# Kernel tuning notes

Hardware: AMD Instinct MI355X
Metric: run time of the kernel (lower is better)

## Reference

```python
import jax, jax.numpy as jnp
import numpy as np

EPS = 1e-5
B, N = 16, 131072

def _bn(x, g, b, m, v):
    # x: [C, N]; inference-mode batchnorm with given stats
    return g[:, None] * (x - m[:, None]) * jax.lax.rsqrt(v[:, None] + EPS) + b[:, None]

def _make_npts():
    base = N // B
    offs = np.linspace(-2048, 2048, B).astype(np.int64)
    npts = np.full(B, base, dtype=np.int64) + offs
    npts[-1] += N - npts.sum()
    assert npts.sum() == N and (npts > 0).all()
    return npts

def setup_inputs() -> dict:
    key = jax.random.key(0)
    ks = jax.random.split(key, 16)
    d = {}
    d["x"] = jax.random.normal(ks[0], (3, N), jnp.float32)
    d["npts"] = jnp.asarray(_make_npts(), jnp.int32)
    def w(k, o, i):
        return jax.random.normal(k, (o, i), jnp.float32) * (1.0 / np.sqrt(i))
    def bnp(k, c):
        k1, k2, k3, k4 = jax.random.split(k, 4)
        return (1.0 + 0.1 * jax.random.normal(k1, (c,), jnp.float32),
                0.1 * jax.random.normal(k2, (c,), jnp.float32),
                0.1 * jax.random.normal(k3, (c,), jnp.float32),
                0.5 + jax.random.uniform(k4, (c,), jnp.float32))
    d["W1"] = w(ks[1], 128, 3);   d["b1"] = jnp.zeros(128, jnp.float32)
    d["g1"], d["be1"], d["m1"], d["v1"] = bnp(ks[2], 128)
    d["W2"] = w(ks[3], 256, 128); d["b2"] = jnp.zeros(256, jnp.float32)
    d["g2"], d["be2"], d["m2"], d["v2"] = bnp(ks[4], 256)
    d["W3"] = w(ks[5], 512, 512); d["b3"] = jnp.zeros(512, jnp.float32)
    d["g3"], d["be3"], d["m3"], d["v3"] = bnp(ks[6], 512)
    d["W4"] = w(ks[7], 1024, 512); d["b4"] = jnp.zeros(1024, jnp.float32)
    d["g4"], d["be4"], d["m4"], d["v4"] = bnp(ks[8], 1024)
    return d

def reference(x, npts,
              W1, b1, g1, be1, m1, v1,
              W2, b2, g2, be2, m2, v2,
              W3, b3, g3, be3, m3, v3,
              W4, b4, g4, be4, m4, v4):
    # segment ids for the ragged point->cloud mapping (replaces torch.split loops)
    seg = jnp.repeat(jnp.arange(B, dtype=jnp.int32), npts, total_repeat_length=N)  # [N]
    h = jax.nn.relu(_bn(W1 @ x + b1[:, None], g1, be1, m1, v1))        # [128, N]
    f = _bn(W2 @ h + b2[:, None], g2, be2, m2, v2)                      # [256, N]
    g = jax.ops.segment_max(f.T, seg, num_segments=B)                   # [B, 256]
    gs = g[seg].T                                                       # [256, N] broadcast back
    xc = jnp.concatenate([gs, f], axis=0)                               # [512, N]
    h3 = jax.nn.relu(_bn(W3 @ xc + b3[:, None], g3, be3, m3, v3))       # [512, N]
    h4 = _bn(W4 @ h3 + b4[:, None], g4, be4, m4, v4)                    # [1024, N]
    v = jax.ops.segment_max(h4.T, seg, num_segments=B)                  # [B, 1024]
    return v
```

## Files before the change

kernel.cpp:

```cpp
#include <hip/hip_runtime.h>
#include <hip/hip_bf16.h>
#include <stdint.h>

#define NTOT 131072
#define NSEG 16
#define EPSV 1e-5f

typedef __attribute__((ext_vector_type(8))) short bf16x8;
typedef __attribute__((ext_vector_type(4))) float f32x4;

struct Args {
  const float* x; const int* npts;
  const float *W1,*b1,*g1,*be1,*m1,*v1;
  const float *W2,*b2,*g2,*be2,*m2,*v2;
  const float *W3,*b3,*g3,*be3,*m3,*v3;
  const float *W4,*b4,*g4,*be4,*m4,*v4;
  int* offs;
  float *a1,*c1,*a2,*c2,*a3,*c3,*a4,*c4;
  unsigned int *gkeys,*vkeys;
  unsigned short *w2b;
  unsigned short *w3p;
  unsigned short *w4p;
  unsigned short *fbufp;
  unsigned short *h3p;
  float* cseg;
  float* out;
};

__device__ inline unsigned int f2key(float f){ unsigned u=__float_as_uint(f); return (u&0x80000000u)? ~u : (u|0x80000000u); }
__device__ inline float key2f(unsigned k){ unsigned u=(k&0x80000000u)? (k^0x80000000u) : ~k; return __uint_as_float(u); }
__device__ inline unsigned short f2bf(float f){ __hip_bfloat16 h=__float2bfloat16(f); return *(unsigned short*)&h; }

__device__ inline void gl16(const void* g, void* l){
  __builtin_amdgcn_global_load_lds((const __attribute__((address_space(1))) unsigned int*)g,
                                   (__attribute__((address_space(3))) unsigned int*)l, 16, 0, 0);
}

__global__ void k_setup(Args A){
  int tid = threadIdx.x;
  if (tid==0){ int s=0; A.offs[0]=0; for (int i=0;i<NSEG;i++){ s+=A.npts[i]; A.offs[i+1]=s; } }
  for (int c=tid;c<128;c+=256){ float a=A.g1[c]*rsqrtf(A.v1[c]+EPSV); A.a1[c]=a; A.c1[c]=A.be1[c]+a*(A.b1[c]-A.m1[c]); }
  for (int c=tid;c<256;c+=256){ float a=A.g2[c]*rsqrtf(A.v2[c]+EPSV); A.a2[c]=a; A.c2[c]=A.be2[c]+a*(A.b2[c]-A.m2[c]); }
  for (int c=tid;c<512;c+=256){ float a=A.g3[c]*rsqrtf(A.v3[c]+EPSV); A.a3[c]=a; A.c3[c]=A.be3[c]+a*(A.b3[c]-A.m3[c]); }
  for (int c=tid;c<1024;c+=256){ float a=A.g4[c]*rsqrtf(A.v4[c]+EPSV); A.a4[c]=a; A.c4[c]=A.be4[c]+a*(A.b4[c]-A.m4[c]); }
  for (int i=tid;i<NSEG*256;i+=256)  A.gkeys[i]=0u;
  for (int i=tid;i<NSEG*1024;i+=256) A.vkeys[i]=0u;
}

__global__ void k_conv(Args A){
  const int n1=256*128;
  const int n2=131072;
  const int n3=524288;
  for (int i = blockIdx.x*256+threadIdx.x; i < n1+n2+n3; i += gridDim.x*256){
    if (i<n1) A.w2b[i]=f2bf(A.W2[i]);
    else if (i<n1+n2){
      int o=i-n1; int j=o&7, cr=(o>>3)&127, kgg=(o>>10)&31, mt=o>>15;
      A.w3p[o]=f2bf(A.W3[(size_t)(mt*128+cr)*512 + 256 + kgg*8 + j]);
    } else {
      int o=i-n1-n2; int j=o&7, cr=(o>>3)&127, kgg=(o>>10)&63, mt=o>>16;
      A.w4p[o]=f2bf(A.W4[(size_t)(mt*128+cr)*512 + kgg*8 + j]);
    }
  }
}

__global__ __launch_bounds__(256) void k_l12(Args A){
  __shared__ float w1s[384], a1s[128], c1s[128], a2s[256], c2s[256];
  __shared__ float xs[3][64];
  __shared__ int offs_s[NSEG+1], segp[64];
  __shared__ unsigned short hs[16*64*8];
  int tid=threadIdx.x, pt0=blockIdx.x*64;
  for (int i=tid;i<384;i+=256) w1s[i]=A.W1[i];
  if (tid<128){ a1s[tid]=A.a1[tid]; c1s[tid]=A.c1[tid]; }
  a2s[tid]=A.a2[tid]; c2s[tid]=A.c2[tid];
  if (tid<=NSEG) offs_s[tid]=A.offs[tid];
  if (tid<64){ xs[0][tid]=A.x[pt0+tid]; xs[1][tid]=A.x[NTOT+pt0+tid]; xs[2][tid]=A.x[2*NTOT+pt0+tid]; }
  __syncthreads();
  if (tid<64){ int gp=pt0+tid, s=0; while (gp>=offs_s[s+1]) s++; segp[tid]=s; }
  for (int pair=tid; pair<1024; pair+=256){
    int pt=pair&63, kc=pair>>6;
    float x0=xs[0][pt], x1=xs[1][pt], x2=xs[2][pt];
    unsigned short us[8];
    #pragma unroll
    for (int j=0;j<8;j++){
      int cin=kc*8+j;
      float v = fmaf(w1s[cin*3],x0, fmaf(w1s[cin*3+1],x1, w1s[cin*3+2]*x2));
      v = fmaxf(fmaf(a1s[cin],v,c1s[cin]), 0.f);
      us[j]=f2bf(v);
    }
    uint4 pk;
    pk.x=(unsigned)us[0]|((unsigned)us[1]<<16); pk.y=(unsigned)us[2]|((unsigned)us[3]<<16);
    pk.z=(unsigned)us[4]|((unsigned)us[5]<<16); pk.w=(unsigned)us[6]|((unsigned)us[7]<<16);
    *(uint4*)(&hs[(kc*64+pt)*8]) = pk;
  }
  __syncthreads();
  int lane=tid&63, wv=tid>>6, quad=lane>>4, l16=lane&15;
  int m0=wv*64;
  f32x4 acc[4][4];
  for (int a=0;a<4;a++)
    for (int b=0;b<4;b++)
      acc[a][b]=(f32x4){0.f,0.f,0.f,0.f};
  #pragma unroll
  for (int ks=0; ks<4; ++ks){
    bf16x8 bfr[4];
    #pragma unroll
    for (int nt=0; nt<4; ++nt) bfr[nt]=*(bf16x8*)(&hs[((ks*4+quad)*64 + nt*16 + l16)*8]);
    #pragma unroll
    for (int mt=0; mt<4; ++mt){
      bf16x8 afr = *(const bf16x8*)(&A.w2b[(m0+mt*16+l16)*128 + ks*32 + quad*8]);
      #pragma unroll
      for (int nt=0; nt<4; ++nt)
        acc[mt][nt]=__builtin_amdgcn_mfma_f32_16x16x32_bf16(afr, bfr[nt], acc[mt][nt], 0,0,0);
    }
  }
  bool uni = (segp[0]==segp[63]); int seg0=segp[0];
  size_t tb = (size_t)(blockIdx.x>>1)*32768;
  int prelb = (blockIdx.x&1)*64;
  #pragma unroll
  for (int mt=0;mt<4;++mt){
    int cout0=m0+mt*16+quad*4;
    int kg=cout0>>3, sub=cout0&7;
    float fv[4][4];
    #pragma unroll
    for (int nt=0;nt<4;++nt)
      #pragma unroll
      for (int r=0;r<4;++r)
        fv[nt][r]=fmaf(a2s[cout0+r], acc[mt][nt][r], c2s[cout0+r]);
    #pragma unroll
    for (int nt=0;nt<4;++nt){
      int ptl=nt*16+l16;
      uint2 pk;
      pk.x=(unsigned)f2bf(fv[nt][0])|((unsigned)f2bf(fv[nt][1])<<16);
      pk.y=(unsigned)f2bf(fv[nt][2])|((unsigned)f2bf(fv[nt][3])<<16);
      *(uint2*)&A.fbufp[tb + (size_t)((kg*128 + prelb + ptl)*8 + sub)] = pk;
    }
    #pragma unroll
    for (int r=0;r<4;++r){
      if (uni){
        float mv=fmaxf(fmaxf(fv[0][r],fv[1][r]),fmaxf(fv[2][r],fv[3][r]));
        #pragma unroll
        for (int off=8;off>=1;off>>=1) mv=fmaxf(mv, __shfl_xor(mv,off));
        if (l16==0) atomicMax(&A.gkeys[seg0*256+cout0+r], f2key(mv));
      } else {
        #pragma unroll
        for (int nt=0;nt<4;++nt)
          atomicMax(&A.gkeys[segp[nt*16+l16]*256+cout0+r], f2key(fv[nt][r]));
      }
    }
  }
}

__global__ void k_cseg(Args A){
  int seg = blockIdx.x>>1; int cout = (blockIdx.x&1)*256 + threadIdx.x;
  __shared__ float gs[256];
  gs[threadIdx.x] = key2f(A.gkeys[seg*256+threadIdx.x]);
  __syncthreads();
  const float* wrow = A.W3 + (size_t)cout*512;
  float s=0.f;
  #pragma unroll 8
  for (int k=0;k<256;k++) s = fmaf(wrow[k], gs[k], s);
  A.cseg[seg*512+cout]=s;
}

__global__ __launch_bounds__(256,4) void k_l3(Args A){
  __shared__ unsigned short sA[8192], sB[8192];
  __shared__ int offs_s[NSEG+1];
  int bid=blockIdx.x, xcd=bid&7, idx=bid>>3;
  int mtile=idx&3, ntile=xcd*128+(idx>>2);
  int tid=threadIdx.x, lane=tid&63, wv=tid>>6, quad=lane>>4, l16=lane&15;
  int mq=wv&1, nq=wv>>1;
  const char* wbase=(const char*)A.w3p   + (size_t)mtile*65536;
  const char* bbase=(const char*)A.fbufp + (size_t)ntile*65536;
  if (tid<=NSEG) offs_s[tid]=A.offs[tid];
  f32x4 acc[4][4];
  for (int a=0;a<4;a++)
    for (int b=0;b<4;b++)
      acc[a][b]=(f32x4){0.f,0.f,0.f,0.f};
  for (int s=0;s<4;++s){
    const char* srcA = wbase + s*16384;
    const char* srcB = bbase + s*16384;
    #pragma unroll
    for (int i=0;i<4;++i){
      gl16(srcA + wv*4096 + i*1024 + lane*16, (char*)sA + wv*4096 + i*1024);
      gl16(srcB + wv*4096 + i*1024 + lane*16, (char*)sB + wv*4096 + i*1024);
    }
    __syncthreads();
    #pragma unroll
    for (int ks=0;ks<2;++ks){
      bf16x8 bb[4], afr[4];
      #pragma unroll
      for (int nt=0;nt<4;++nt) bb[nt]=*(const bf16x8*)(&sB[((ks*4+quad)*128 + nq*64 + nt*16 + l16)*8]);
      #pragma unroll
      for (int mt=0;mt<4;++mt) afr[mt]=*(const bf16x8*)(&sA[((ks*4+quad)*128 + mq*64 + mt*16 + l16)*8]);
      #pragma unroll
      for (int mt=0;mt<4;++mt)
        #pragma unroll
        for (int nt=0;nt<4;++nt)
          acc[mt][nt]=__builtin_amdgcn_mfma_f32_16x16x32_bf16(afr[mt], bb[nt], acc[mt][nt], 0,0,0);
    }
    __syncthreads();
  }
  int pt0 = ntile*128 + nq*64;
  int sBeg=0; while (pt0 >= offs_s[sBeg+1]) sBeg++;
  int sEnd=sBeg; while (pt0+63 >= offs_s[sEnd+1]) sEnd++;
  bool uni=(sBeg==sEnd);
  int segl[4];
  if (!uni){
    #pragma unroll
    for (int nt=0;nt<4;++nt){ int gp=pt0+nt*16+l16, ss=sBeg; while (gp>=offs_s[ss+1]) ss++; segl[nt]=ss; }
  }
  size_t hb = (size_t)ntile*65536;
  #pragma unroll
  for (int mt=0;mt<4;++mt){
    int cout0=mtile*128 + mq*64 + mt*16 + quad*4;
    int kg=cout0>>3, sub=cout0&7;
    float sa[4],sc[4],csr[4];
    #pragma unroll
    for (int r=0;r<4;++r){ sa[r]=A.a3[cout0+r]; sc[r]=A.c3[cout0+r]; }
    if (uni){
      #pragma unroll
      for (int r=0;r<4;++r) csr[r]=A.cseg[sBeg*512+cout0+r];
    }
    #pragma unroll
    for (int nt=0;nt<4;++nt){
      int prel=nq*64+nt*16+l16;
      unsigned short us[4];
      #pragma unroll
      for (int r=0;r<4;++r){
        float cv = uni? csr[r] : A.cseg[segl[nt]*512+cout0+r];
        float hv = fmaxf(fmaf(sa[r], acc[mt][nt][r]+cv, sc[r]), 0.f);
        us[r]=f2bf(hv);
      }
      uint2 pk;
      pk.x=(unsigned)us[0]|((unsigned)us[1]<<16);
      pk.y=(unsigned)us[2]|((unsigned)us[3]<<16);
      *(uint2*)&A.h3p[hb + (size_t)((kg*128+prel)*8+sub)] = pk;
    }
  }
}

__global__ __launch_bounds__(256,4) void k_l4(Args A){
  __shared__ unsigned short sA[8192], sB[8192];
  __shared__ int offs_s[NSEG+1];
  int bid=blockIdx.x, xcd=bid&7, idx=bid>>3;
  int mtile=idx&7, ntile=xcd*128+(idx>>3);
  int tid=threadIdx.x, lane=tid&63, wv=tid>>6, quad=lane>>4, l16=lane&15;
  int mq=wv&1, nq=wv>>1;
  const char* wbase=(const char*)A.w4p + (size_t)mtile*131072;
  const char* bbase=(const char*)A.h3p + (size_t)ntile*131072;
  if (tid<=NSEG) offs_s[tid]=A.offs[tid];
  f32x4 acc[4][4];
  for (int a=0;a<4;a++)
    for (int b=0;b<4;b++)
      acc[a][b]=(f32x4){0.f,0.f,0.f,0.f};
  for (int s=0;s<8;++s){
    const char* srcA = wbase + s*16384;
    const char* srcB = bbase + s*16384;
    #pragma unroll
    for (int i=0;i<4;++i){
      gl16(srcA + wv*4096 + i*1024 + lane*16, (char*)sA + wv*4096 + i*1024);
      gl16(srcB + wv*4096 + i*1024 + lane*16, (char*)sB + wv*4096 + i*1024);
    }
    __syncthreads();
    #pragma unroll
    for (int ks=0;ks<2;++ks){
      bf16x8 bb[4], afr[4];
      #pragma unroll
      for (int nt=0;nt<4;++nt) bb[nt]=*(const bf16x8*)(&sB[((ks*4+quad)*128 + nq*64 + nt*16 + l16)*8]);
      #pragma unroll
      for (int mt=0;mt<4;++mt) afr[mt]=*(const bf16x8*)(&sA[((ks*4+quad)*128 + mq*64 + mt*16 + l16)*8]);
      #pragma unroll
      for (int mt=0;mt<4;++mt)
        #pragma unroll
        for (int nt=0;nt<4;++nt)
          acc[mt][nt]=__builtin_amdgcn_mfma_f32_16x16x32_bf16(afr[mt], bb[nt], acc[mt][nt], 0,0,0);
    }
    __syncthreads();
  }
  int pt0 = ntile*128 + nq*64;
  int sBeg=0; while (pt0 >= offs_s[sBeg+1]) sBeg++;
  int sEnd=sBeg; while (pt0+63 >= offs_s[sEnd+1]) sEnd++;
  bool uni=(sBeg==sEnd);
  int segl[4];
  if (!uni){
    #pragma unroll
    for (int nt=0;nt<4;++nt){ int gp=pt0+nt*16+l16, ss=sBeg; while (gp>=offs_s[ss+1]) ss++; segl[nt]=ss; }
  }
  #pragma unroll
  for (int mt=0;mt<4;++mt){
    int cout0=mtile*128 + mq*64 + mt*16 + quad*4;
    #pragma unroll
    for (int r=0;r<4;++r){
      int cout=cout0+r;
      float sa=A.a4[cout], sc=A.c4[cout];
      float mv=-3.4e38f;
      #pragma unroll
      for (int nt=0;nt<4;++nt){
        float fv=fmaf(sa, acc[mt][nt][r], sc);
        if (uni) mv=fmaxf(mv,fv);
        else atomicMax(&A.vkeys[segl[nt]*1024+cout], f2key(fv));
      }
      if (uni){
        #pragma unroll
        for (int off=8;off>=1;off>>=1) mv=fmaxf(mv, __shfl_xor(mv,off));
        if (l16==0) atomicMax(&A.vkeys[sBeg*1024+cout], f2key(mv));
      }
    }
  }
}

__global__ void k_final(Args A){
  int i=blockIdx.x*256+threadIdx.x;
  if (i<NSEG*1024) A.out[i]=key2f(A.vkeys[i]);
}

extern "C" void kernel_launch(void* const* d_in, const int* in_sizes, int n_in,
                              void* d_out, int out_size, void* d_ws, size_t ws_size,
                              hipStream_t stream){
  Args A;
  A.x  =(const float*)d_in[0];  A.npts=(const int*)d_in[1];
  A.W1 =(const float*)d_in[2];  A.b1 =(const float*)d_in[3];
  A.g1 =(const float*)d_in[4];  A.be1=(const float*)d_in[5];
  A.m1 =(const float*)d_in[6];  A.v1 =(const float*)d_in[7];
  A.W2 =(const float*)d_in[8];  A.b2 =(const float*)d_in[9];
  A.g2 =(const float*)d_in[10]; A.be2=(const float*)d_in[11];
  A.m2 =(const float*)d_in[12]; A.v2 =(const float*)d_in[13];
  A.W3 =(const float*)d_in[14]; A.b3 =(const float*)d_in[15];
  A.g3 =(const float*)d_in[16]; A.be3=(const float*)d_in[17];
  A.m3 =(const float*)d_in[18]; A.v3 =(const float*)d_in[19];
  A.W4 =(const float*)d_in[20]; A.b4 =(const float*)d_in[21];
  A.g4 =(const float*)d_in[22]; A.be4=(const float*)d_in[23];
  A.m4 =(const float*)d_in[24]; A.v4 =(const float*)d_in[25];

  char* w=(char*)d_ws;
  auto alloc=[&](size_t b)->void*{ void* p=(void*)w; w += (b+255)&~(size_t)255; return p; };
  A.offs =(int*)alloc((NSEG+1)*4);
  A.a1=(float*)alloc(128*4);  A.c1=(float*)alloc(128*4);
  A.a2=(float*)alloc(256*4);  A.c2=(float*)alloc(256*4);
  A.a3=(float*)alloc(512*4);  A.c3=(float*)alloc(512*4);
  A.a4=(float*)alloc(1024*4); A.c4=(float*)alloc(1024*4);
  A.gkeys=(unsigned int*)alloc(NSEG*256*4);
  A.vkeys=(unsigned int*)alloc(NSEG*1024*4);
  A.cseg =(float*)alloc(NSEG*512*4);
  A.w2b=(unsigned short*)alloc(256*128*2);
  A.w3p=(unsigned short*)alloc(131072*2);
  A.w4p=(unsigned short*)alloc(524288*2);
  A.fbufp=(unsigned short*)alloc((size_t)1024*32768*2);
  A.h3p  =(unsigned short*)alloc((size_t)1024*65536*2);
  A.out=(float*)d_out;

  k_setup<<<dim3(1),dim3(256),0,stream>>>(A);
  k_conv <<<dim3(2688),dim3(256),0,stream>>>(A);
  k_l12  <<<dim3(NTOT/64),dim3(256),0,stream>>>(A);
  k_cseg <<<dim3(32),dim3(256),0,stream>>>(A);
  k_l3   <<<dim3(4096),dim3(256),0,stream>>>(A);
  k_l4   <<<dim3(8192),dim3(256),0,stream>>>(A);
  k_final<<<dim3(64),dim3(256),0,stream>>>(A);
}
```

Measured before the change: 604.2 us.

## Enlarge layer-3/4 GEMM block tile to 256 output channels with 8 waves

The layer-3 and layer-4 MFMA GEMM kernels now use 512-thread blocks that each compute a 256x128 output tile instead of 128x128, and the packed weight layout is changed to match. Each staged activation tile is reused across twice as many output channels, cutting global and L2 traffic for the large activation operand and halving the block count. The cost is more LDS per block and fewer resident blocks per CU (launch bounds 512,2), which could reduce latency hiding.

```diff
diff --git a/kernel.cpp b/kernel.cpp
--- a/kernel.cpp
+++ b/kernel.cpp
@@ -54,11 +54,11 @@
   for (int i = blockIdx.x*256+threadIdx.x; i < n1+n2+n3; i += gridDim.x*256){
     if (i<n1) A.w2b[i]=f2bf(A.W2[i]);
     else if (i<n1+n2){
-      int o=i-n1; int j=o&7, cr=(o>>3)&127, kgg=(o>>10)&31, mt=o>>15;
-      A.w3p[o]=f2bf(A.W3[(size_t)(mt*128+cr)*512 + 256 + kgg*8 + j]);
+      int o=i-n1; int j=o&7, cr=(o>>3)&255; int g=o>>11; int kgg=g&7, kt=(g>>3)&3, Mt=g>>5;
+      A.w3p[o]=f2bf(A.W3[(size_t)(Mt*256+cr)*512 + 256 + kt*64 + kgg*8 + j]);
     } else {
-      int o=i-n1-n2; int j=o&7, cr=(o>>3)&127, kgg=(o>>10)&63, mt=o>>16;
-      A.w4p[o]=f2bf(A.W4[(size_t)(mt*128+cr)*512 + kgg*8 + j]);
+      int o=i-n1-n2; int j=o&7, cr=(o>>3)&255; int g=o>>11; int kgg=g&7, kt=(g>>3)&7, Mt=g>>6;
+      A.w4p[o]=f2bf(A.W4[(size_t)(Mt*256+cr)*512 + kt*64 + kgg*8 + j]);
     }
   }
 }
@@ -161,14 +161,14 @@
   A.cseg[seg*512+cout]=s;
 }
 
-__global__ __launch_bounds__(256,4) void k_l3(Args A){
-  __shared__ unsigned short sA[8192], sB[8192];
+__global__ __launch_bounds__(512,2) void k_l3(Args A){
+  __shared__ unsigned short sA[16384], sB[8192];
   __shared__ int offs_s[NSEG+1];
   int bid=blockIdx.x, xcd=bid&7, idx=bid>>3;
-  int mtile=idx&3, ntile=xcd*128+(idx>>2);
+  int Mt=idx&1, ntile=xcd*128+(idx>>1);
   int tid=threadIdx.x, lane=tid&63, wv=tid>>6, quad=lane>>4, l16=lane&15;
-  int mq=wv&1, nq=wv>>1;
-  const char* wbase=(const char*)A.w3p   + (size_t)mtile*65536;
+  int wm=wv>>1, wn=wv&1;
+  const char* wbase=(const char*)A.w3p   + (size_t)Mt*131072;
   const char* bbase=(const char*)A.fbufp + (size_t)ntile*65536;
   if (tid<=NSEG) offs_s[tid]=A.offs[tid];
   f32x4 acc[4][4];
@@ -176,21 +176,22 @@
     for (int b=0;b<4;b++)
       acc[a][b]=(f32x4){0.f,0.f,0.f,0.f};
   for (int s=0;s<4;++s){
-    const char* srcA = wbase + s*16384;
+    const char* srcA = wbase + s*32768;
     const char* srcB = bbase + s*16384;
     #pragma unroll
-    for (int i=0;i<4;++i){
+    for (int i=0;i<4;++i)
       gl16(srcA + wv*4096 + i*1024 + lane*16, (char*)sA + wv*4096 + i*1024);
-      gl16(srcB + wv*4096 + i*1024 + lane*16, (char*)sB + wv*4096 + i*1024);
-    }
+    #pragma unroll
+    for (int i=0;i<2;++i)
+      gl16(srcB + wv*2048 + i*1024 + lane*16, (char*)sB + wv*2048 + i*1024);
     __syncthreads();
     #pragma unroll
     for (int ks=0;ks<2;++ks){
       bf16x8 bb[4], afr[4];
       #pragma unroll
-      for (int nt=0;nt<4;++nt) bb[nt]=*(const bf16x8*)(&sB[((ks*4+quad)*128 + nq*64 + nt*16 + l16)*8]);
-      #pragma unroll
-      for (int mt=0;mt<4;++mt) afr[mt]=*(const bf16x8*)(&sA[((ks*4+quad)*128 + mq*64 + mt*16 + l16)*8]);
+      for (int nt=0;nt<4;++nt) bb[nt]=*(const bf16x8*)(&sB[((ks*4+quad)*128 + wn*64 + nt*16 + l16)*8]);
+      #pragma unroll
+      for (int mt=0;mt<4;++mt) afr[mt]=*(const bf16x8*)(&sA[((ks*4+quad)*256 + wm*64 + mt*16 + l16)*8]);
       #pragma unroll
       for (int mt=0;mt<4;++mt)
         #pragma unroll
@@ -199,7 +200,7 @@
     }
     __syncthreads();
   }
-  int pt0 = ntile*128 + nq*64;
+  int pt0 = ntile*128 + wn*64;
   int sBeg=0; while (pt0 >= offs_s[sBeg+1]) sBeg++;
   int sEnd=sBeg; while (pt0+63 >= offs_s[sEnd+1]) sEnd++;
   bool uni=(sBeg==sEnd);
@@ -211,7 +212,7 @@
   size_t hb = (size_t)ntile*65536;
   #pragma unroll
   for (int mt=0;mt<4;++mt){
-    int cout0=mtile*128 + mq*64 + mt*16 + quad*4;
+    int cout0=Mt*256 + wm*64 + mt*16 + quad*4;
     int kg=cout0>>3, sub=cout0&7;
     float sa[4],sc[4],csr[4];
     #pragma unroll
@@ -222,7 +223,7 @@
     }
     #pragma unroll
     for (int nt=0;nt<4;++nt){
-      int prel=nq*64+nt*16+l16;
+      int prel=wn*64+nt*16+l16;
       unsigned short us[4];
       #pragma unroll
       for (int r=0;r<4;++r){
@@ -238,14 +239,14 @@
   }
 }
 
-__global__ __launch_bounds__(256,4) void k_l4(Args A){
-  __shared__ unsigned short sA[8192], sB[8192];
+__global__ __launch_bounds__(512,2) void k_l4(Args A){
+  __shared__ unsigned short sA[16384], sB[8192];
   __shared__ int offs_s[NSEG+1];
   int bid=blockIdx.x, xcd=bid&7, idx=bid>>3;
-  int mtile=idx&7, ntile=xcd*128+(idx>>3);
+  int Mt=idx&3, ntile=xcd*128+(idx>>2);
   int tid=threadIdx.x, lane=tid&63, wv=tid>>6, quad=lane>>4, l16=lane&15;
-  int mq=wv&1, nq=wv>>1;
-  const char* wbase=(const char*)A.w4p + (size_t)mtile*131072;
+  int wm=wv>>1, wn=wv&1;
+  const char* wbase=(const char*)A.w4p + (size_t)Mt*262144;
   const char* bbase=(const char*)A.h3p + (size_t)ntile*131072;
   if (tid<=NSEG) offs_s[tid]=A.offs[tid];
   f32x4 acc[4][4];
@@ -253,21 +254,22 @@
     for (int b=0;b<4;b++)
       acc[a][b]=(f32x4){0.f,0.f,0.f,0.f};
   for (int s=0;s<8;++s){
-    const char* srcA = wbase + s*16384;
+    const char* srcA = wbase + s*32768;
     const char* srcB = bbase + s*16384;
     #pragma unroll
-    for (int i=0;i<4;++i){
+    for (int i=0;i<4;++i)
       gl16(srcA + wv*4096 + i*1024 + lane*16, (char*)sA + wv*4096 + i*1024);
-      gl16(srcB + wv*4096 + i*1024 + lane*16, (char*)sB + wv*4096 + i*1024);
-    }
+    #pragma unroll
+    for (int i=0;i<2;++i)
+      gl16(srcB + wv*2048 + i*1024 + lane*16, (char*)sB + wv*2048 + i*1024);
     __syncthreads();
     #pragma unroll
     for (int ks=0;ks<2;++ks){
       bf16x8 bb[4], afr[4];
       #pragma unroll
-      for (int nt=0;nt<4;++nt) bb[nt]=*(const bf16x8*)(&sB[((ks*4+quad)*128 + nq*64 + nt*16 + l16)*8]);
-      #pragma unroll
-      for (int mt=0;mt<4;++mt) afr[mt]=*(const bf16x8*)(&sA[((ks*4+quad)*128 + mq*64 + mt*16 + l16)*8]);
+      for (int nt=0;nt<4;++nt) bb[nt]=*(const bf16x8*)(&sB[((ks*4+quad)*128 + wn*64 + nt*16 + l16)*8]);
+      #pragma unroll
+      for (int mt=0;mt<4;++mt) afr[mt]=*(const bf16x8*)(&sA[((ks*4+quad)*256 + wm*64 + mt*16 + l16)*8]);
       #pragma unroll
       for (int mt=0;mt<4;++mt)
         #pragma unroll
@@ -276,7 +278,7 @@
     }
     __syncthreads();
   }
-  int pt0 = ntile*128 + nq*64;
+  int pt0 = ntile*128 + wn*64;
   int sBeg=0; while (pt0 >= offs_s[sBeg+1]) sBeg++;
   int sEnd=sBeg; while (pt0+63 >= offs_s[sEnd+1]) sEnd++;
   bool uni=(sBeg==sEnd);
@@ -287,7 +289,7 @@
   }
   #pragma unroll
   for (int mt=0;mt<4;++mt){
-    int cout0=mtile*128 + mq*64 + mt*16 + quad*4;
+    int cout0=Mt*256 + wm*64 + mt*16 + quad*4;
     #pragma unroll
     for (int r=0;r<4;++r){
       int cout=cout0+r;
@@ -352,7 +354,7 @@
   k_conv <<<dim3(2688),dim3(256),0,stream>>>(A);
   k_l12  <<<dim3(NTOT/64),dim3(256),0,stream>>>(A);
   k_cseg <<<dim3(32),dim3(256),0,stream>>>(A);
-  k_l3   <<<dim3(4096),dim3(256),0,stream>>>(A);
-  k_l4   <<<dim3(8192),dim3(256),0,stream>>>(A);
+  k_l3   <<<dim3(2048),dim3(512),0,stream>>>(A);
+  k_l4   <<<dim3(4096),dim3(512),0,stream>>>(A);
   k_final<<<dim3(64),dim3(256),0,stream>>>(A);
 }
```

New measurement: 620.7 us. 2.7% more time.
